# Kernel tuning notes

Hardware: AMD Instinct MI355X
Metric: run time of the kernel (lower is better)

## Reference

```python
import jax, jax.numpy as jnp
import numpy as np

BETA = 1.0
ALPHA = 0.5


def setup_inputs() -> dict:
    key = jax.random.key(0)
    k1, k2, k3 = jax.random.split(key, 3)
    B, N1, N2 = 512, 256, 32768
    v = jax.random.normal(k1, (B, N1), dtype=jnp.float32)
    mask = jax.random.uniform(k2, (B, N1), dtype=jnp.float32)
    Mem = jax.random.normal(k3, (N2, N1), dtype=jnp.float32)  # kernel [N2, N1] (trailing 1 squeezed)
    return {"v": v, "mask": mask, "Mem": Mem}


def reference(v, mask, Mem):
    # Squared L2 distance d2[i, b] = ||Mem[i] - v[b]||^2, computed without the
    # [N2, N1, B] diff tensor via the expansion ||m||^2 - 2 m.v + ||v||^2.
    m2 = jnp.sum(Mem * Mem, axis=1)            # [N2]
    v2 = jnp.sum(v * v, axis=1)                # [B]
    cross = jnp.einsum('nd,bd->nb', Mem, v)    # [N2, B]
    d2 = m2[:, None] - 2.0 * cross + v2[None, :]
    # Gaussian-kernel weights over the N2 stored patterns (softmax == exp/sum).
    w = jax.nn.softmax(-0.5 * BETA * d2, axis=0)  # [N2, B]
    # update[b] = sum_i w[i,b] * (Mem[i] - v[b]) = (w^T Mem)[b] - v[b]
    update = jnp.einsum('nb,nd->bd', w, Mem) - v   # [B, N1]
    return v + ALPHA * update * mask
```

## Files before the change

kernel.cpp:

```cpp
#include <hip/hip_runtime.h>
#include <hip/hip_bf16.h>
#include <stdint.h>

typedef float  f32x4 __attribute__((ext_vector_type(4)));
typedef _Float16 half8 __attribute__((ext_vector_type(8)));
typedef unsigned int uint32;

#define N1 256
#define N2T 32768
#define BQ 512
#define KT 32
#define TILE_B 16384

#define RA_OFF 0
#define MT_OFF 32768
#define P_OFF  65536
#define P_PITCH 80
#define P_WSTR  2560
#define LDS_BYTES 75776

union H4 { _Float16 h[4]; unsigned short s[4]; uint2 u2; };

#define GLD_LDS(gp, lp) __builtin_amdgcn_global_load_lds( \
    (const __attribute__((address_space(1))) void*)(gp), \
    (__attribute__((address_space(3))) void*)(lp), 16, 0, 0)

__global__ __launch_bounds__(256) void mhn_prep_k(
    const float* __restrict__ Mem, _Float16* __restrict__ MemA,
    _Float16* __restrict__ MemT, float* __restrict__ m2g)
{
  const int t   = blockIdx.x;
  const int tid = threadIdx.x;
  const int a    = tid >> 4;
  const int dblk = tid & 15;
  const int r0i  = 32*t + 2*a;

  const float* p0 = Mem + (size_t)r0i*N1 + dblk*16;
  const float* p1 = p0 + N1;
  float4 x0[4], x1[4];
  #pragma unroll
  for (int i=0;i<4;i++){ x0[i] = *(const float4*)(p0+4*i); x1[i] = *(const float4*)(p1+4*i); }

  float s0=0.f, s1=0.f;
  H4 h0[4], h1[4];
  #pragma unroll
  for (int i=0;i<4;i++){
    s0 += x0[i].x*x0[i].x + x0[i].y*x0[i].y + x0[i].z*x0[i].z + x0[i].w*x0[i].w;
    s1 += x1[i].x*x1[i].x + x1[i].y*x1[i].y + x1[i].z*x1[i].z + x1[i].w*x1[i].w;
    h0[i].h[0]=(_Float16)x0[i].x; h0[i].h[1]=(_Float16)x0[i].y; h0[i].h[2]=(_Float16)x0[i].z; h0[i].h[3]=(_Float16)x0[i].w;
    h1[i].h[0]=(_Float16)x1[i].x; h1[i].h[1]=(_Float16)x1[i].y; h1[i].h[2]=(_Float16)x1[i].z; h1[i].h[3]=(_Float16)x1[i].w;
  }

  char* bA = (char*)MemA + (size_t)t*TILE_B;
  {
    const int e0 = (2*a)&7, e1 = (2*a+1)&7;
    uint4 wv;
    wv.x=h0[0].u2.x; wv.y=h0[0].u2.y; wv.z=h0[1].u2.x; wv.w=h0[1].u2.y;
    *(uint4*)(bA + (2*a)*512   + (((2*dblk  )^e0)<<4)) = wv;
    wv.x=h0[2].u2.x; wv.y=h0[2].u2.y; wv.z=h0[3].u2.x; wv.w=h0[3].u2.y;
    *(uint4*)(bA + (2*a)*512   + (((2*dblk+1)^e0)<<4)) = wv;
    wv.x=h1[0].u2.x; wv.y=h1[0].u2.y; wv.z=h1[1].u2.x; wv.w=h1[1].u2.y;
    *(uint4*)(bA + (2*a+1)*512 + (((2*dblk  )^e1)<<4)) = wv;
    wv.x=h1[2].u2.x; wv.y=h1[2].u2.y; wv.z=h1[3].u2.x; wv.w=h1[3].u2.y;
    *(uint4*)(bA + (2*a+1)*512 + (((2*dblk+1)^e1)<<4)) = wv;
  }

  char* bT = (char*)MemT + (size_t)t*TILE_B;
  #pragma unroll
  for (int i=0;i<4;i++){
    #pragma unroll
    for (int j=0;j<4;j++){
      const int d = dblk*16 + 4*i + j;
      const uint32 pk = (uint32)h0[i].s[j] | ((uint32)h1[i].s[j] << 16);
      *(uint32*)(bT + d*64 + ((((a>>2) ^ ((d>>1)&3)))<<4) + ((a&3)<<2)) = pk;
    }
  }

  s0 += __shfl_xor(s0,1); s0 += __shfl_xor(s0,2); s0 += __shfl_xor(s0,4); s0 += __shfl_xor(s0,8);
  s1 += __shfl_xor(s1,1); s1 += __shfl_xor(s1,2); s1 += __shfl_xor(s1,4); s1 += __shfl_xor(s1,8);
  if (dblk == 0){ m2g[r0i] = -0.5f*s0; m2g[r0i+1] = -0.5f*s1; }
}

__global__ __launch_bounds__(256, 2) void mhn_flash_k(
    const _Float16* __restrict__ MemA, const _Float16* __restrict__ MemT,
    const float* __restrict__ m2g, const float* __restrict__ v,
    __hip_bfloat16* __restrict__ Opart, float* __restrict__ mpart,
    float* __restrict__ lpart, int CK, int nt)
{
  __shared__ __align__(16) char lds[LDS_BYTES];

  const int tid = threadIdx.x;
  const int w  = tid >> 6;
  const int l  = tid & 63;
  const int lg = l >> 4;
  const int lc = l & 15;

  const int nwg = gridDim.x;
  const int bid = blockIdx.x;
  const int s_  = (bid & 7) * (nwg >> 3) + (bid >> 3);
  const int c   = s_ >> 2;
  const int qb  = s_ & 3;

  auto dma = [&](int tt, int bw){
    const size_t off = (size_t)(c*(CK>>5) + tt)*TILE_B + w*4096 + l*16;
    const char* gA = (const char*)MemA + off;
    const char* gT = (const char*)MemT + off;
    char* dA = lds + RA_OFF + bw*TILE_B + w*4096 + l*16;
    char* dT = lds + MT_OFF + bw*TILE_B + w*4096 + l*16;
    #pragma unroll
    for (int i=0;i<4;i++){
      GLD_LDS(gA + i*1024, dA + i*1024);
      GLD_LDS(gT + i*1024, dT + i*1024);
    }
  };

  dma(0, 0);

  half8 v8a[8], v8b[8];
  {
    const int qg = qb*128 + w*32 + lc;
    const float* vp0 = v + (size_t)qg*N1 + lg*8;
    const float* vp1 = vp0 + 16*N1;
    #pragma unroll
    for (int s=0;s<8;s++){
      float4 a = *(const float4*)(vp0 + 32*s), b = *(const float4*)(vp0 + 32*s + 4);
      half8 hv;
      hv[0]=(_Float16)a.x; hv[1]=(_Float16)a.y; hv[2]=(_Float16)a.z; hv[3]=(_Float16)a.w;
      hv[4]=(_Float16)b.x; hv[5]=(_Float16)b.y; hv[6]=(_Float16)b.z; hv[7]=(_Float16)b.w;
      v8a[s]=hv;
      a = *(const float4*)(vp1 + 32*s); b = *(const float4*)(vp1 + 32*s + 4);
      hv[0]=(_Float16)a.x; hv[1]=(_Float16)a.y; hv[2]=(_Float16)a.z; hv[3]=(_Float16)a.w;
      hv[4]=(_Float16)b.x; hv[5]=(_Float16)b.y; hv[6]=(_Float16)b.z; hv[7]=(_Float16)b.w;
      v8b[s]=hv;
    }
  }

  float mrun0=-INFINITY, mrun1=-INFINITY, lrun0=0.f, lrun1=0.f;
  f32x4 oA[16], oB[16];
  #pragma unroll
  for (int df=0;df<16;df++){ oA[df]=(f32x4){0,0,0,0}; oB[df]=(f32x4){0,0,0,0}; }

  __syncthreads();

  const int x7  = lc & 7;
  const int lcx = (lc >> 1) & 3;

  for (int tt=0; tt<nt; ++tt){
    const int buf = tt & 1;
    const bool pf = (tt+1 < nt);
    if (pf) dma(tt+1, buf^1);

    const float* m2p = m2g + c*CK + tt*KT;
    const f32x4 m2a = *(const f32x4*)(m2p + 4*lg);
    const f32x4 m2b = *(const f32x4*)(m2p + 16 + 4*lg);

    const char* ra = lds + RA_OFF + buf*TILE_B;
    f32x4 sA0={0,0,0,0}, sB0={0,0,0,0}, sA1={0,0,0,0}, sB1={0,0,0,0};
    #pragma unroll
    for (int s=0;s<8;s++){
      const int g = ((s<<2)|lg) ^ x7;
      const half8 a0 = *(const half8*)(ra + lc*512      + (g<<4));
      const half8 a1 = *(const half8*)(ra + (16+lc)*512 + (g<<4));
      sA0 = __builtin_amdgcn_mfma_f32_16x16x32_f16(a0, v8a[s], sA0, 0,0,0);
      sB0 = __builtin_amdgcn_mfma_f32_16x16x32_f16(a1, v8a[s], sB0, 0,0,0);
      sA1 = __builtin_amdgcn_mfma_f32_16x16x32_f16(a0, v8b[s], sA1, 0,0,0);
      sB1 = __builtin_amdgcn_mfma_f32_16x16x32_f16(a1, v8b[s], sB1, 0,0,0);
    }
    sA0 += m2a; sB0 += m2b; sA1 += m2a; sB1 += m2b;

    float tm0 = fmaxf(fmaxf(fmaxf(sA0[0],sA0[1]),fmaxf(sA0[2],sA0[3])),
                      fmaxf(fmaxf(sB0[0],sB0[1]),fmaxf(sB0[2],sB0[3])));
    float tm1 = fmaxf(fmaxf(fmaxf(sA1[0],sA1[1]),fmaxf(sA1[2],sA1[3])),
                      fmaxf(fmaxf(sB1[0],sB1[1]),fmaxf(sB1[2],sB1[3])));
    tm0 = fmaxf(tm0, __shfl_xor(tm0,16)); tm0 = fmaxf(tm0, __shfl_xor(tm0,32));
    tm1 = fmaxf(tm1, __shfl_xor(tm1,16)); tm1 = fmaxf(tm1, __shfl_xor(tm1,32));
    if (__any((tm0 > mrun0 + 8.0f) || (tm1 > mrun1 + 8.0f))){
      const float nm0 = fmaxf(mrun0, tm0), nm1 = fmaxf(mrun1, tm1);
      const float sc0 = __expf(mrun0 - nm0), sc1 = __expf(mrun1 - nm1);
      lrun0 *= sc0; lrun1 *= sc1; mrun0 = nm0; mrun1 = nm1;
      const int b0 = __float_as_int(sc0), b1 = __float_as_int(sc1);
      f32x4 scv0, scv1;
      #pragma unroll
      for (int r2=0;r2<4;r2++){
        scv0[r2] = __int_as_float(__builtin_amdgcn_ds_bpermute((4*lg+r2)<<2, b0));
        scv1[r2] = __int_as_float(__builtin_amdgcn_ds_bpermute((4*lg+r2)<<2, b1));
      }
      #pragma unroll
      for (int df=0;df<16;df++){ oA[df] *= scv0; oB[df] *= scv1; }
    }
    H4 k0,k1,k2,k3;
    k0.h[0]=(_Float16)__expf(sA0[0]-mrun0); k0.h[1]=(_Float16)__expf(sA0[1]-mrun0);
    k0.h[2]=(_Float16)__expf(sA0[2]-mrun0); k0.h[3]=(_Float16)__expf(sA0[3]-mrun0);
    k1.h[0]=(_Float16)__expf(sB0[0]-mrun0); k1.h[1]=(_Float16)__expf(sB0[1]-mrun0);
    k1.h[2]=(_Float16)__expf(sB0[2]-mrun0); k1.h[3]=(_Float16)__expf(sB0[3]-mrun0);
    k2.h[0]=(_Float16)__expf(sA1[0]-mrun1); k2.h[1]=(_Float16)__expf(sA1[1]-mrun1);
    k2.h[2]=(_Float16)__expf(sA1[2]-mrun1); k2.h[3]=(_Float16)__expf(sA1[3]-mrun1);
    k3.h[0]=(_Float16)__expf(sB1[0]-mrun1); k3.h[1]=(_Float16)__expf(sB1[1]-mrun1);
    k3.h[2]=(_Float16)__expf(sB1[2]-mrun1); k3.h[3]=(_Float16)__expf(sB1[3]-mrun1);
    float ps0 = ((float)k0.h[0]+(float)k0.h[1])+((float)k0.h[2]+(float)k0.h[3])
              + ((float)k1.h[0]+(float)k1.h[1])+((float)k1.h[2]+(float)k1.h[3]);
    float ps1 = ((float)k2.h[0]+(float)k2.h[1])+((float)k2.h[2]+(float)k2.h[3])
              + ((float)k3.h[0]+(float)k3.h[1])+((float)k3.h[2]+(float)k3.h[3]);
    ps0 += __shfl_xor(ps0,16); ps0 += __shfl_xor(ps0,32); lrun0 += ps0;
    ps1 += __shfl_xor(ps1,16); ps1 += __shfl_xor(ps1,32); lrun1 += ps1;

    char* pw = lds + P_OFF + w*P_WSTR;
    *(uint2*)(pw + lc*P_PITCH + lg*8)           = k0.u2;
    *(uint2*)(pw + lc*P_PITCH + 32 + lg*8)      = k1.u2;
    *(uint2*)(pw + (16+lc)*P_PITCH + lg*8)      = k2.u2;
    *(uint2*)(pw + (16+lc)*P_PITCH + 32 + lg*8) = k3.u2;
    const half8 pa0 = *(const half8*)(pw + lc*P_PITCH + lg*16);
    const half8 pa1 = *(const half8*)(pw + (16+lc)*P_PITCH + lg*16);

    const char* mtb = lds + MT_OFF + buf*TILE_B + lc*64 + ((lg ^ lcx) << 4);
    #pragma unroll
    for (int df=0; df<16; df++){
      const half8 bb = *(const half8*)(mtb + df*1024);
      oA[df] = __builtin_amdgcn_mfma_f32_16x16x32_f16(pa0, bb, oA[df], 0,0,0);
      oB[df] = __builtin_amdgcn_mfma_f32_16x16x32_f16(pa1, bb, oB[df], 0,0,0);
    }

    __syncthreads();
  }

  __hip_bfloat16* Op = Opart + (size_t)c*BQ*N1;
  const int q0 = qb*128 + w*32 + 4*lg;
  #pragma unroll
  for (int df=0; df<16; df++){
    #pragma unroll
    for (int r2=0;r2<4;r2++){
      Op[(size_t)(q0+r2)*N1    + df*16 + lc] = __float2bfloat16(oA[df][r2]);
      Op[(size_t)(q0+16+r2)*N1 + df*16 + lc] = __float2bfloat16(oB[df][r2]);
    }
  }
  if (lg == 0){
    const int qq = qb*128 + w*32 + lc;
    mpart[(size_t)c*BQ + qq]      = mrun0;
    lpart[(size_t)c*BQ + qq]      = lrun0;
    mpart[(size_t)c*BQ + qq + 16] = mrun1;
    lpart[(size_t)c*BQ + qq + 16] = lrun1;
  }
}

__global__ __launch_bounds__(256) void mhn_reduce_k(
    const float* __restrict__ v, const float* __restrict__ mask,
    const __hip_bfloat16* __restrict__ Opart, const float* __restrict__ mpart,
    const float* __restrict__ lpart, float* __restrict__ out, int nchunk)
{
  __shared__ float msh[256], lsh[256];
  const int q = blockIdx.x, tid = threadIdx.x;
  if (tid < nchunk){
    msh[tid] = mpart[(size_t)tid*BQ + q];
    lsh[tid] = lpart[(size_t)tid*BQ + q];
  }
  __syncthreads();
  float M = -INFINITY;
  for (int c2=0;c2<nchunk;c2++) M = fmaxf(M, msh[c2]);
  float L = 0.f, o = 0.f;
  for (int c2=0;c2<nchunk;c2++){
    const float e = __expf(msh[c2] - M);
    L += lsh[c2]*e;
    o += __bfloat162float(Opart[((size_t)c2*BQ + q)*N1 + tid])*e;
  }
  const float vv = v[q*N1+tid], mk = mask[q*N1+tid];
  out[q*N1+tid] = vv + 0.5f*((o/L) - vv)*mk;
}

extern "C" void kernel_launch(void* const* d_in, const int* in_sizes, int n_in,
                              void* d_out, int out_size, void* d_ws, size_t ws_size,
                              hipStream_t stream)
{
  (void)in_sizes; (void)n_in; (void)out_size;
  const float* v    = (const float*)d_in[0];
  const float* mask = (const float*)d_in[1];
  const float* Mem  = (const float*)d_in[2];
  float* out = (float*)d_out;

  const size_t fixedB   = (size_t)N2T*N1*2*2 + (size_t)N2T*4;
  const size_t perChunk = (size_t)BQ*N1*2 + (size_t)BQ*8;
  int nchunk = 128;
  while (nchunk > 4 && fixedB + (size_t)nchunk*perChunk > ws_size) nchunk >>= 1;

  char* wsb = (char*)d_ws;
  _Float16* MemA = (_Float16*)wsb;
  _Float16* MemT = (_Float16*)(wsb + (size_t)N2T*N1*2);
  float*    m2g  = (float*)(wsb + (size_t)N2T*N1*4);
  char* pb = wsb + fixedB;
  __hip_bfloat16* Opart = (__hip_bfloat16*)pb;
  float* mpart = (float*)(pb + (size_t)nchunk*BQ*N1*2);
  float* lpart = mpart + (size_t)nchunk*BQ;

  const int CK = N2T / nchunk;
  const int nt = CK / KT;

  mhn_prep_k<<<dim3(N2T/KT), dim3(256), 0, stream>>>(Mem, MemA, MemT, m2g);
  mhn_flash_k<<<dim3(4*nchunk), dim3(256), 0, stream>>>(MemA, MemT, m2g, v, Opart, mpart, lpart, CK, nt);
  mhn_reduce_k<<<dim3(BQ), dim3(256), 0, stream>>>(v, mask, Opart, mpart, lpart, out, nchunk);
}
```

Before: 77.63 us.

## Switch flash kernel to 32x32x16 MFMA with register-shuffled P operand

```diff
diff --git a/kernel.cpp b/kernel.cpp
--- a/kernel.cpp
+++ b/kernel.cpp
@@ -2,7 +2,8 @@
 #include <hip/hip_bf16.h>
 #include <stdint.h>
 
-typedef float  f32x4 __attribute__((ext_vector_type(4)));
+typedef float  f32x4  __attribute__((ext_vector_type(4)));
+typedef float  f32x16 __attribute__((ext_vector_type(16)));
 typedef _Float16 half8 __attribute__((ext_vector_type(8)));
 typedef unsigned int uint32;
 
@@ -14,10 +15,7 @@
 
 #define RA_OFF 0
 #define MT_OFF 32768
-#define P_OFF  65536
-#define P_PITCH 80
-#define P_WSTR  2560
-#define LDS_BYTES 75776
+#define LDS_BYTES 65536
 
 union H4 { _Float16 h[4]; unsigned short s[4]; uint2 u2; };
 
@@ -90,10 +88,10 @@
   __shared__ __align__(16) char lds[LDS_BYTES];
 
   const int tid = threadIdx.x;
-  const int w  = tid >> 6;
-  const int l  = tid & 63;
-  const int lg = l >> 4;
-  const int lc = l & 15;
+  const int w   = tid >> 6;
+  const int l   = tid & 63;
+  const int row = l & 31;
+  const int hi  = l >> 5;
 
   const int nwg = gridDim.x;
   const int bid = blockIdx.x;
@@ -116,34 +114,32 @@
 
   dma(0, 0);
 
-  half8 v8a[8], v8b[8];
+  half8 v8[16];
+  const int q0 = qb*128 + w*32;
   {
-    const int qg = qb*128 + w*32 + lc;
-    const float* vp0 = v + (size_t)qg*N1 + lg*8;
-    const float* vp1 = vp0 + 16*N1;
-    #pragma unroll
-    for (int s=0;s<8;s++){
-      float4 a = *(const float4*)(vp0 + 32*s), b = *(const float4*)(vp0 + 32*s + 4);
+    const float* vp = v + (size_t)(q0 + row)*N1 + 8*hi;
+    #pragma unroll
+    for (int s=0;s<16;s++){
+      const float4 a = *(const float4*)(vp + 16*s);
+      const float4 b = *(const float4*)(vp + 16*s + 4);
       half8 hv;
       hv[0]=(_Float16)a.x; hv[1]=(_Float16)a.y; hv[2]=(_Float16)a.z; hv[3]=(_Float16)a.w;
       hv[4]=(_Float16)b.x; hv[5]=(_Float16)b.y; hv[6]=(_Float16)b.z; hv[7]=(_Float16)b.w;
-      v8a[s]=hv;
-      a = *(const float4*)(vp1 + 32*s); b = *(const float4*)(vp1 + 32*s + 4);
-      hv[0]=(_Float16)a.x; hv[1]=(_Float16)a.y; hv[2]=(_Float16)a.z; hv[3]=(_Float16)a.w;
-      hv[4]=(_Float16)b.x; hv[5]=(_Float16)b.y; hv[6]=(_Float16)b.z; hv[7]=(_Float16)b.w;
-      v8b[s]=hv;
-    }
-  }
-
-  float mrun0=-INFINITY, mrun1=-INFINITY, lrun0=0.f, lrun1=0.f;
-  f32x4 oA[16], oB[16];
-  #pragma unroll
-  for (int df=0;df<16;df++){ oA[df]=(f32x4){0,0,0,0}; oB[df]=(f32x4){0,0,0,0}; }
+      v8[s]=hv;
+    }
+  }
+
+  float mrun = -INFINITY, lrun = 0.f;
+  f32x16 oacc[8];
+  #pragma unroll
+  for (int b=0;b<8;b++) oacc[b] = (f32x16)(0.f);
+
+  const int e7 = row & 7;
+  const uint32 qkB = (uint32)(row*512 + ((hi ^ (e7 & 1)) << 4) + ((e7 >> 1) << 5));
+  const int sd = (row >> 1) & 3;
+  const uint32 pvB = (uint32)(row*64 + ((hi ^ (sd & 1)) << 4) + ((sd >> 1) << 5));
 
   __syncthreads();
-
-  const int x7  = lc & 7;
-  const int lcx = (lc >> 1) & 3;
 
   for (int tt=0; tt<nt; ++tt){
     const int buf = tt & 1;
@@ -151,119 +147,115 @@
     if (pf) dma(tt+1, buf^1);
 
     const float* m2p = m2g + c*CK + tt*KT;
-    const f32x4 m2a = *(const f32x4*)(m2p + 4*lg);
-    const f32x4 m2b = *(const f32x4*)(m2p + 16 + 4*lg);
+    f32x4 m2v[4];
+    #pragma unroll
+    for (int b=0;b<4;b++) m2v[b] = *(const f32x4*)(m2p + 8*b + 4*hi);
 
     const char* ra = lds + RA_OFF + buf*TILE_B;
-    f32x4 sA0={0,0,0,0}, sB0={0,0,0,0}, sA1={0,0,0,0}, sB1={0,0,0,0};
-    #pragma unroll
-    for (int s=0;s<8;s++){
-      const int g = ((s<<2)|lg) ^ x7;
-      const half8 a0 = *(const half8*)(ra + lc*512      + (g<<4));
-      const half8 a1 = *(const half8*)(ra + (16+lc)*512 + (g<<4));
-      sA0 = __builtin_amdgcn_mfma_f32_16x16x32_f16(a0, v8a[s], sA0, 0,0,0);
-      sB0 = __builtin_amdgcn_mfma_f32_16x16x32_f16(a1, v8a[s], sB0, 0,0,0);
-      sA1 = __builtin_amdgcn_mfma_f32_16x16x32_f16(a0, v8b[s], sA1, 0,0,0);
-      sB1 = __builtin_amdgcn_mfma_f32_16x16x32_f16(a1, v8b[s], sB1, 0,0,0);
-    }
-    sA0 += m2a; sB0 += m2b; sA1 += m2a; sB1 += m2b;
-
-    float tm0 = fmaxf(fmaxf(fmaxf(sA0[0],sA0[1]),fmaxf(sA0[2],sA0[3])),
-                      fmaxf(fmaxf(sB0[0],sB0[1]),fmaxf(sB0[2],sB0[3])));
-    float tm1 = fmaxf(fmaxf(fmaxf(sA1[0],sA1[1]),fmaxf(sA1[2],sA1[3])),
-                      fmaxf(fmaxf(sB1[0],sB1[1]),fmaxf(sB1[2],sB1[3])));
-    tm0 = fmaxf(tm0, __shfl_xor(tm0,16)); tm0 = fmaxf(tm0, __shfl_xor(tm0,32));
-    tm1 = fmaxf(tm1, __shfl_xor(tm1,16)); tm1 = fmaxf(tm1, __shfl_xor(tm1,32));
-    if (__any((tm0 > mrun0 + 8.0f) || (tm1 > mrun1 + 8.0f))){
-      const float nm0 = fmaxf(mrun0, tm0), nm1 = fmaxf(mrun1, tm1);
-      const float sc0 = __expf(mrun0 - nm0), sc1 = __expf(mrun1 - nm1);
-      lrun0 *= sc0; lrun1 *= sc1; mrun0 = nm0; mrun1 = nm1;
-      const int b0 = __float_as_int(sc0), b1 = __float_as_int(sc1);
-      f32x4 scv0, scv1;
+    f32x16 S = (f32x16)(0.f);
+    #pragma unroll
+    for (int s=0;s<16;s++){
+      const half8 a = *(const half8*)(ra + (qkB ^ (uint32)(s<<5)));
+      S = __builtin_amdgcn_mfma_f32_32x32x16_f16(a, v8[s], S, 0,0,0);
+    }
+
+    float p[16];
+    #pragma unroll
+    for (int r=0;r<16;r++) p[r] = S[r] + m2v[r>>2][r&3];
+
+    float tm = p[0];
+    #pragma unroll
+    for (int r=1;r<16;r++) tm = fmaxf(tm, p[r]);
+    tm = fmaxf(tm, __shfl_xor(tm, 32));
+    if (__any(tm > mrun + 8.0f)){
+      const float nm = fmaxf(mrun, tm);
+      const float sc = __expf(mrun - nm);
+      lrun *= sc; mrun = nm;
       #pragma unroll
-      for (int r2=0;r2<4;r2++){
-        scv0[r2] = __int_as_float(__builtin_amdgcn_ds_bpermute((4*lg+r2)<<2, b0));
-        scv1[r2] = __int_as_float(__builtin_amdgcn_ds_bpermute((4*lg+r2)<<2, b1));
+      for (int b=0;b<8;b++) oacc[b] *= sc;
+    }
+    #pragma unroll
+    for (int r=0;r<16;r++) p[r] = __expf(p[r] - mrun);
+    float ps = 0.f;
+    #pragma unroll
+    for (int r=0;r<16;r++) ps += p[r];
+    ps += __shfl_xor(ps, 32); lrun += ps;
+
+    uint32 D[8];
+    #pragma unroll
+    for (int i=0;i<8;i++){
+      union { __fp16 h2 __attribute__((ext_vector_type(2))); uint32 u; } cv;
+      cv.h2 = __builtin_amdgcn_cvt_pkrtz(p[2*i], p[2*i+1]);
+      D[i] = cv.u;
+    }
+    uint32 wq[8];
+    {
+      const uint32 tD0 = (uint32)__shfl_xor((int)D[0], 32);
+      const uint32 tD1 = (uint32)__shfl_xor((int)D[1], 32);
+      const uint32 tD2 = (uint32)__shfl_xor((int)D[2], 32);
+      const uint32 tD3 = (uint32)__shfl_xor((int)D[3], 32);
+      const uint32 tD4 = (uint32)__shfl_xor((int)D[4], 32);
+      const uint32 tD5 = (uint32)__shfl_xor((int)D[5], 32);
+      const uint32 tD6 = (uint32)__shfl_xor((int)D[6], 32);
+      const uint32 tD7 = (uint32)__shfl_xor((int)D[7], 32);
+      const bool lo = (hi == 0);
+      wq[0] = lo ? D[0] : tD2;  wq[1] = lo ? D[1] : tD3;
+      wq[2] = lo ? tD0 : D[2];  wq[3] = lo ? tD1 : D[3];
+      wq[4] = lo ? D[4] : tD6;  wq[5] = lo ? D[5] : tD7;
+      wq[6] = lo ? tD4 : D[6];  wq[7] = lo ? tD5 : D[7];
+    }
+    union { uint32 u[4]; half8 h; } pb1, pb2;
+    pb1.u[0]=wq[0]; pb1.u[1]=wq[1]; pb1.u[2]=wq[2]; pb1.u[3]=wq[3];
+    pb2.u[0]=wq[4]; pb2.u[1]=wq[5]; pb2.u[2]=wq[6]; pb2.u[3]=wq[7];
+
+    const char* mtb = lds + MT_OFF + buf*TILE_B;
+    const char* a1 = (const char*)(mtb + pvB);
+    const char* a2 = (const char*)(mtb + (pvB ^ 32u));
+    #pragma unroll
+    for (int b=0;b<8;b++){
+      const half8 A1 = *(const half8*)(a1 + b*2048);
+      oacc[b] = __builtin_amdgcn_mfma_f32_32x32x16_f16(A1, pb1.h, oacc[b], 0,0,0);
+      const half8 A2 = *(const half8*)(a2 + b*2048);
+      oacc[b] = __builtin_amdgcn_mfma_f32_32x32x16_f16(A2, pb2.h, oacc[b], 0,0,0);
+    }
+
+    __syncthreads();
+  }
+
+  {
+    __hip_bfloat16* Op = Opart + (size_t)c*N1*BQ + (q0 + row);
+    #pragma unroll
+    for (int b=0;b<8;b++){
+      #pragma unroll
+      for (int r=0;r<16;r++){
+        const int d = 32*b + (r&3) + 8*(r>>2) + 4*hi;
+        Op[(size_t)d*BQ] = __float2bfloat16(oacc[b][r]);
       }
-      #pragma unroll
-      for (int df=0;df<16;df++){ oA[df] *= scv0; oB[df] *= scv1; }
-    }
-    H4 k0,k1,k2,k3;
-    k0.h[0]=(_Float16)__expf(sA0[0]-mrun0); k0.h[1]=(_Float16)__expf(sA0[1]-mrun0);
-    k0.h[2]=(_Float16)__expf(sA0[2]-mrun0); k0.h[3]=(_Float16)__expf(sA0[3]-mrun0);
-    k1.h[0]=(_Float16)__expf(sB0[0]-mrun0); k1.h[1]=(_Float16)__expf(sB0[1]-mrun0);
-    k1.h[2]=(_Float16)__expf(sB0[2]-mrun0); k1.h[3]=(_Float16)__expf(sB0[3]-mrun0);
-    k2.h[0]=(_Float16)__expf(sA1[0]-mrun1); k2.h[1]=(_Float16)__expf(sA1[1]-mrun1);
-    k2.h[2]=(_Float16)__expf(sA1[2]-mrun1); k2.h[3]=(_Float16)__expf(sA1[3]-mrun1);
-    k3.h[0]=(_Float16)__expf(sB1[0]-mrun1); k3.h[1]=(_Float16)__expf(sB1[1]-mrun1);
-    k3.h[2]=(_Float16)__expf(sB1[2]-mrun1); k3.h[3]=(_Float16)__expf(sB1[3]-mrun1);
-    float ps0 = ((float)k0.h[0]+(float)k0.h[1])+((float)k0.h[2]+(float)k0.h[3])
-              + ((float)k1.h[0]+(float)k1.h[1])+((float)k1.h[2]+(float)k1.h[3]);
-    float ps1 = ((float)k2.h[0]+(float)k2.h[1])+((float)k2.h[2]+(float)k2.h[3])
-              + ((float)k3.h[0]+(float)k3.h[1])+((float)k3.h[2]+(float)k3.h[3]);
-    ps0 += __shfl_xor(ps0,16); ps0 += __shfl_xor(ps0,32); lrun0 += ps0;
-    ps1 += __shfl_xor(ps1,16); ps1 += __shfl_xor(ps1,32); lrun1 += ps1;
-
-    char* pw = lds + P_OFF + w*P_WSTR;
-    *(uint2*)(pw + lc*P_PITCH + lg*8)           = k0.u2;
-    *(uint2*)(pw + lc*P_PITCH + 32 + lg*8)      = k1.u2;
-    *(uint2*)(pw + (16+lc)*P_PITCH + lg*8)      = k2.u2;
-    *(uint2*)(pw + (16+lc)*P_PITCH + 32 + lg*8) = k3.u2;
-    const half8 pa0 = *(const half8*)(pw + lc*P_PITCH + lg*16);
-    const half8 pa1 = *(const half8*)(pw + (16+lc)*P_PITCH + lg*16);
-
-    const char* mtb = lds + MT_OFF + buf*TILE_B + lc*64 + ((lg ^ lcx) << 4);
-    #pragma unroll
-    for (int df=0; df<16; df++){
-      const half8 bb = *(const half8*)(mtb + df*1024);
-      oA[df] = __builtin_amdgcn_mfma_f32_16x16x32_f16(pa0, bb, oA[df], 0,0,0);
-      oB[df] = __builtin_amdgcn_mfma_f32_16x16x32_f16(pa1, bb, oB[df], 0,0,0);
-    }
-
-    __syncthreads();
-  }
-
-  __hip_bfloat16* Op = Opart + (size_t)c*BQ*N1;
-  const int q0 = qb*128 + w*32 + 4*lg;
-  #pragma unroll
-  for (int df=0; df<16; df++){
-    #pragma unroll
-    for (int r2=0;r2<4;r2++){
-      Op[(size_t)(q0+r2)*N1    + df*16 + lc] = __float2bfloat16(oA[df][r2]);
-      Op[(size_t)(q0+16+r2)*N1 + df*16 + lc] = __float2bfloat16(oB[df][r2]);
-    }
-  }
-  if (lg == 0){
-    const int qq = qb*128 + w*32 + lc;
-    mpart[(size_t)c*BQ + qq]      = mrun0;
-    lpart[(size_t)c*BQ + qq]      = lrun0;
-    mpart[(size_t)c*BQ + qq + 16] = mrun1;
-    lpart[(size_t)c*BQ + qq + 16] = lrun1;
-  }
-}
-
-__global__ __launch_bounds__(256) void mhn_reduce_k(
+    }
+    if (hi == 0){
+      mpart[(size_t)c*BQ + q0 + row] = mrun;
+      lpart[(size_t)c*BQ + q0 + row] = lrun;
+    }
+  }
+}
+
+__global__ __launch_bounds__(512) void mhn_reduce_k(
     const float* __restrict__ v, const float* __restrict__ mask,
     const __hip_bfloat16* __restrict__ Opart, const float* __restrict__ mpart,
     const float* __restrict__ lpart, float* __restrict__ out, int nchunk)
 {
-  __shared__ float msh[256], lsh[256];
-  const int q = blockIdx.x, tid = threadIdx.x;
-  if (tid < nchunk){
-    msh[tid] = mpart[(size_t)tid*BQ + q];
-    lsh[tid] = lpart[(size_t)tid*BQ + q];
-  }
-  __syncthreads();
+  const int d = blockIdx.x;
+  const int q = threadIdx.x;
   float M = -INFINITY;
-  for (int c2=0;c2<nchunk;c2++) M = fmaxf(M, msh[c2]);
+  for (int c2=0;c2<nchunk;c2++) M = fmaxf(M, mpart[(size_t)c2*BQ + q]);
   float L = 0.f, o = 0.f;
   for (int c2=0;c2<nchunk;c2++){
-    const float e = __expf(msh[c2] - M);
-    L += lsh[c2]*e;
-    o += __bfloat162float(Opart[((size_t)c2*BQ + q)*N1 + tid])*e;
-  }
-  const float vv = v[q*N1+tid], mk = mask[q*N1+tid];
-  out[q*N1+tid] = vv + 0.5f*((o/L) - vv)*mk;
+    const float e = __expf(mpart[(size_t)c2*BQ + q] - M);
+    L += lpart[(size_t)c2*BQ + q]*e;
+    o += __bfloat162float(Opart[((size_t)c2*N1 + d)*BQ + q])*e;
+  }
+  const float vv = v[(size_t)q*N1 + d], mk = mask[(size_t)q*N1 + d];
+  out[(size_t)q*N1 + d] = vv + 0.5f*((o/L) - vv)*mk;
 }
 
 extern "C" void kernel_launch(void* const* d_in, const int* in_sizes, int n_in,
@@ -295,5 +287,5 @@
 
   mhn_prep_k<<<dim3(N2T/KT), dim3(256), 0, stream>>>(Mem, MemA, MemT, m2g);
   mhn_flash_k<<<dim3(4*nchunk), dim3(256), 0, stream>>>(MemA, MemT, m2g, v, Opart, mpart, lpart, CK, nt);
-  mhn_reduce_k<<<dim3(BQ), dim3(256), 0, stream>>>(v, mask, Opart, mpart, lpart, out, nchunk);
-}
+  mhn_reduce_k<<<dim3(N1), dim3(BQ), 0, stream>>>(v, mask, Opart, mpart, lpart, out, nchunk);
+}
```

Measured after the change: 110.3 us. +42.1%, slower.
